# Performance work log

Measured on AMD Instinct MI355X. Metric: run time of the kernel, lower is better.

Reference implementation:

```python
import jax, jax.numpy as jnp
import numpy as np
import math

D_MODEL = 1024
N_HEAD = 16


def setup_inputs() -> dict:
    key = jax.random.key(0)
    ks = jax.random.split(key, 5)
    x = jax.random.normal(ks[0], (2, 2048, D_MODEL), dtype=jnp.float32)
    # Linear params (torch Linear: y = x @ W.T + b); store as [in, out] for einsum
    s1 = 1.0 / math.sqrt(D_MODEL)
    W_qkv = jax.random.uniform(ks[1], (D_MODEL, 3 * D_MODEL), jnp.float32, -s1, s1)
    b_qkv = jax.random.uniform(ks[2], (3 * D_MODEL,), jnp.float32, -s1, s1)
    W_out = jax.random.uniform(ks[3], (D_MODEL, D_MODEL), jnp.float32, -s1, s1)
    b_out = jax.random.uniform(ks[4], (D_MODEL,), jnp.float32, -s1, s1)
    return {"x": x, "W_qkv": W_qkv, "b_qkv": b_qkv, "W_out": W_out, "b_out": b_out}


def reference(x, W_qkv, b_qkv, W_out, b_out):
    B, L, D = x.shape
    H = N_HEAD
    hd = D // H
    qkv = x @ W_qkv + b_qkv                      # [B, L, 3D]
    q, k, v = jnp.split(qkv, 3, axis=-1)
    # [B, H, L, hd]
    q = q.reshape(B, L, H, hd).transpose(0, 2, 1, 3)
    k = k.reshape(B, L, H, hd).transpose(0, 2, 1, 3)
    v = v.reshape(B, L, H, hd).transpose(0, 2, 1, 3)
    scale = 1.0 / math.sqrt(hd)
    scores = jnp.einsum('bhqd,bhkd->bhqk', q, k) * scale   # [B, H, L, L]
    causal = jnp.tril(jnp.ones((L, L), dtype=bool))
    scores = jnp.where(causal, scores, jnp.float32(-jnp.inf))
    probs = jax.nn.softmax(scores, axis=-1)
    out = jnp.einsum('bhqk,bhkd->bhqd', probs, v)          # [B, H, L, hd]
    out = out.transpose(0, 2, 1, 3).reshape(B, L, D)
    out = out @ W_out + b_out
    return jnp.squeeze(out)
```

## Files before the change

kernel.cpp:

```cpp
#include <hip/hip_runtime.h>
#include <hip/hip_bf16.h>

#define SEQ    2048
#define NHEAD  16
#define HD     64
#define DMODEL 1024

using bf16 = __hip_bfloat16;
using short8 = __attribute__((ext_vector_type(8))) short;
using short4v = __attribute__((ext_vector_type(4))) short;
using f32x4  = __attribute__((ext_vector_type(4))) float;

__device__ __forceinline__ float fast_exp2(float x) {
  return __builtin_amdgcn_exp2f(x);
}
#define WAIT_LGKM0() __builtin_amdgcn_s_waitcnt(0xC07F)

__device__ __forceinline__ void gload_lds16(const bf16* g, bf16* l) {
  __builtin_amdgcn_global_load_lds(
      (const __attribute__((address_space(1))) void*)g,
      (__attribute__((address_space(3))) void*)l, 16, 0, 0);
}

__global__ void convert_k(const float* __restrict__ src, bf16* __restrict__ dst,
                          int n) {
  int i = (blockIdx.x * blockDim.x + threadIdx.x) * 8;
  if (i >= n) return;
  bf16 tmp[8];
  #pragma unroll
  for (int j = 0; j < 8; ++j) tmp[j] = __float2bfloat16(src[i + j]);
  *(short8*)&dst[i] = *(short8*)tmp;
}

__global__ void transpose_cvt_k(const float* __restrict__ in, bf16* __restrict__ out,
                                int R, int C) {
  __shared__ bf16 tile[32][33];
  int c0 = blockIdx.x * 32, r0 = blockIdx.y * 32;
  int tx = threadIdx.x & 31, ty = threadIdx.x >> 5;
  #pragma unroll
  for (int i = ty; i < 32; i += 8)
    tile[i][tx] = __float2bfloat16(in[(size_t)(r0 + i) * C + c0 + tx]);
  __syncthreads();
  #pragma unroll
  for (int i = ty; i < 32; i += 8)
    out[(size_t)(c0 + i) * R + r0 + tx] = tile[tx][i];
}

__global__ void transpose_v_k(const bf16* __restrict__ in, bf16* __restrict__ out) {
  __shared__ bf16 tile[32][33];
  const int bh = blockIdx.z;
  const bf16* ip = in  + (size_t)bh * SEQ * HD;
  bf16* op       = out + (size_t)bh * HD * SEQ;
  int c0 = blockIdx.x * 32, r0 = blockIdx.y * 32;
  int tx = threadIdx.x & 31, ty = threadIdx.x >> 5;
  #pragma unroll
  for (int i = ty; i < 32; i += 8)
    tile[i][tx] = ip[(size_t)(r0 + i) * HD + c0 + tx];
  __syncthreads();
  #pragma unroll
  for (int i = ty; i < 32; i += 8)
    op[(size_t)(c0 + i) * SEQ + r0 + tx] = tile[tx][i];
}

template <int MODE>
__global__ __launch_bounds__(256)
void gemm_bt(const bf16* __restrict__ A, const bf16* __restrict__ BT,
             const float* __restrict__ bias,
             bf16* __restrict__ out0, bf16* __restrict__ out1,
             bf16* __restrict__ out2, float* __restrict__ outf) {
  constexpr int K = 1024;
  __shared__ __align__(16) bf16 As[128 * 32];
  __shared__ __align__(16) bf16 Bs[128 * 32];
  const int tid = threadIdx.x;
  const int wave = tid >> 6, lane = tid & 63;
  const int quad = lane >> 4, l16 = lane & 15;
  const int waveM = (wave >> 1) * 64, waveN = (wave & 1) * 64;
  const int m0 = blockIdx.x * 128, n0 = blockIdx.y * 128;
  const int srow = (lane >> 2);
  const int scol = (lane & 3) * 8;

  const f32x4 zero4 = {0.f, 0.f, 0.f, 0.f};
  f32x4 acc[4][4];
  #pragma unroll
  for (int i = 0; i < 4; ++i)
    #pragma unroll
    for (int j = 0; j < 4; ++j) acc[i][j] = zero4;

  for (int k0 = 0; k0 < K; k0 += 32) {
    __syncthreads();
    #pragma unroll
    for (int half = 0; half < 2; ++half) {
      int grow = half * 64 + wave * 16 + srow;
      gload_lds16(&A [(size_t)(m0 + grow) * K + k0 + scol],
                  &As[(half * 64 + wave * 16) * 32]);
      gload_lds16(&BT[(size_t)(n0 + grow) * K + k0 + scol],
                  &Bs[(half * 64 + wave * 16) * 32]);
    }
    __syncthreads();
    short8 af[4], bfm[4];
    #pragma unroll
    for (int mt = 0; mt < 4; ++mt)
      af[mt] = *(const short8*)&As[(waveM + mt * 16 + l16) * 32 + quad * 8];
    #pragma unroll
    for (int nt = 0; nt < 4; ++nt)
      bfm[nt] = *(const short8*)&Bs[(waveN + nt * 16 + l16) * 32 + quad * 8];
    #pragma unroll
    for (int mt = 0; mt < 4; ++mt)
      #pragma unroll
      for (int nt = 0; nt < 4; ++nt)
        acc[mt][nt] = __builtin_amdgcn_mfma_f32_16x16x32_bf16(
            af[mt], bfm[nt], acc[mt][nt], 0, 0, 0);
  }

  #pragma unroll
  for (int nt = 0; nt < 4; ++nt) {
    int n = n0 + waveN + nt * 16 + l16;
    float bvv = bias[n];
    #pragma unroll
    for (int mt = 0; mt < 4; ++mt) {
      #pragma unroll
      for (int r = 0; r < 4; ++r) {
        int m = m0 + waveM + mt * 16 + quad * 4 + r;
        float v = acc[mt][nt][r] + bvv;
        if (MODE == 1) {
          outf[(size_t)m * 1024 + n] = v;
        } else {
          bf16 v16 = __float2bfloat16(v);
          int which = n >> 10, oo = n & 1023;
          int h = oo >> 6, c = oo & 63;
          int b = m >> 11, l = m & 2047;
          size_t idx = ((size_t)(b * NHEAD + h) * SEQ + l) * HD + c;
          if (which == 0)      out0[idx] = v16;
          else if (which == 1) out1[idx] = v16;
          else                 out2[idx] = v16;
        }
      }
    }
  }
}

__global__ __launch_bounds__(256)
void attn_k(const bf16* __restrict__ Q, const bf16* __restrict__ Kb,
            const bf16* __restrict__ VT, bf16* __restrict__ O) {
  __shared__ __align__(16) bf16 Ks[2 * 128 * 32];
  __shared__ __align__(16) bf16 Vs[4 * 64 * 32];
  __shared__ __align__(16) bf16 Plds[4][16][136];
  const int tid = threadIdx.x;
  const int wave = tid >> 6, lane = tid & 63;
  const int quad = lane >> 4, l16 = lane & 15;
  const int srow = lane >> 2, scol = (lane & 3) * 8;
  const int id = blockIdx.x;
  const int bh = id & 31, blkx = id >> 5;
  const int b = bh >> 4, h = bh & 15;

  const bf16* Qp = Q  + (size_t)bh * SEQ * HD;
  const bf16* Kp = Kb + (size_t)bh * SEQ * HD;
  const bf16* Vp = VT + (size_t)bh * HD * SEQ;

  const f32x4 zero4 = {0.f, 0.f, 0.f, 0.f};
  const float c = 0.18033688011112042f;
  const float mc = 8.0f * c;

  #pragma unroll
  for (int pass = 0; pass < 2; ++pass) {
    const int qt = pass ? (31 - blkx) : blkx;
    const int q0w = qt * 64 + wave * 16;
    const int q_lane = q0w + l16;
    const int ntiles = (qt + 2) >> 1;

    short8 qf0 = *(const short8*)&Qp[(size_t)(q0w + l16) * HD + quad * 8];
    short8 qf1 = *(const short8*)&Qp[(size_t)(q0w + l16) * HD + 32 + quad * 8];

    f32x4 oacc[4];
    #pragma unroll
    for (int dt = 0; dt < 4; ++dt) oacc[dt] = zero4;
    float l4[4] = {0.f, 0.f, 0.f, 0.f};

    for (int t = 0; t < ntiles; ++t) {
      const int k0 = t << 7;
      __syncthreads();
      #pragma unroll
      for (int i = 0; i < 2; ++i) {
        int r = wave * 32 + i * 16;
        #pragma unroll
        for (int hh = 0; hh < 2; ++hh)
          gload_lds16(&Kp[(size_t)(k0 + r + srow) * HD + hh * 32 + scol],
                      &Ks[hh * 4096 + r * 32]);
      }
      #pragma unroll
      for (int g = 0; g < 4; ++g)
        gload_lds16(&Vp[(size_t)(g * 16 + srow) * SEQ + k0 + wave * 32 + scol],
                    &Vs[wave * 2048 + g * 16 * 32]);
      __syncthreads();

      f32x4 s[8];
      #pragma unroll
      for (int g = 0; g < 8; ++g) {
        short8 ka = *(const short8*)&Ks[(g * 16 + l16) * 32 + quad * 8];
        short8 kb = *(const short8*)&Ks[4096 + (g * 16 + l16) * 32 + quad * 8];
        f32x4 sg = zero4;
        sg = __builtin_amdgcn_mfma_f32_16x16x32_bf16(ka, qf0, sg, 0, 0, 0);
        sg = __builtin_amdgcn_mfma_f32_16x16x32_bf16(kb, qf1, sg, 0, 0, 0);
        s[g] = sg;
      }

      if (t == ntiles - 1) {
        #pragma unroll
        for (int g = 0; g < 8; ++g)
          #pragma unroll
          for (int r = 0; r < 4; ++r) {
            int k = k0 + g * 16 + quad * 4 + r;
            s[g][r] = (k <= q_lane) ? s[g][r] : -__builtin_inff();
          }
      }

      #pragma unroll
      for (int g = 0; g < 8; ++g) {
        bf16 pb[4];
        #pragma unroll
        for (int r = 0; r < 4; ++r) {
          float p = fast_exp2(__builtin_fmaf(s[g][r], c, -mc));
          l4[r] += p;
          pb[r] = __float2bfloat16(p);
        }
        *(short4v*)&Plds[wave][l16][g * 16 + quad * 4] = *(short4v*)pb;
      }
      WAIT_LGKM0();

      short8 pf[4];
      #pragma unroll
      for (int ch = 0; ch < 4; ++ch)
        pf[ch] = *(const short8*)&Plds[wave][l16][ch * 32 + quad * 8];
      #pragma unroll
      for (int ch = 0; ch < 4; ++ch)
        #pragma unroll
        for (int dt = 0; dt < 4; ++dt) {
          short8 vf = *(const short8*)&Vs[ch * 2048 + (dt * 16 + l16) * 32 + quad * 8];
          oacc[dt] = __builtin_amdgcn_mfma_f32_16x16x32_bf16(vf, pf[ch], oacc[dt], 0, 0, 0);
        }
    }

    float l_i = (l4[0] + l4[1]) + (l4[2] + l4[3]);
    l_i += __shfl_xor(l_i, 16, 64);
    l_i += __shfl_xor(l_i, 32, 64);
    float inv = 1.f / l_i;

    #pragma unroll
    for (int dt = 0; dt < 4; ++dt) {
      bf16 ob[4];
      #pragma unroll
      for (int r = 0; r < 4; ++r) ob[r] = __float2bfloat16(oacc[dt][r] * inv);
      *(short4v*)&Plds[wave][l16][dt * 16 + quad * 4] = *(short4v*)ob;
    }
    WAIT_LGKM0();
    {
      int row = lane >> 2;
      int col = (lane & 3) * 16;
      short8 o0 = *(const short8*)&Plds[wave][row][col];
      short8 o1 = *(const short8*)&Plds[wave][row][col + 8];
      size_t base = ((size_t)(b * SEQ + q0w + row)) * DMODEL + h * HD + col;
      *(short8*)&O[base]     = o0;
      *(short8*)&O[base + 8] = o1;
    }
  }
}

extern "C" void kernel_launch(void* const* d_in, const int* in_sizes, int n_in,
                              void* d_out, int out_size, void* d_ws, size_t ws_size,
                              hipStream_t stream) {
  const float* x    = (const float*)d_in[0];
  const float* Wqkv = (const float*)d_in[1];
  const float* bqkv = (const float*)d_in[2];
  const float* Wout = (const float*)d_in[3];
  const float* bout = (const float*)d_in[4];
  float* out = (float*)d_out;

  char* ws = (char*)d_ws;
  const size_t MB = 1024 * 1024;
  char* big    = ws + 16384;
  bf16* Kbuf   = (bf16*)(big);
  bf16* VTb    = (bf16*)(big + 8 * MB);
  bf16* xb     = (bf16*)(big + 16 * MB);
  bf16* AO     = (bf16*)(big + 16 * MB);
  bf16* WqkvT  = (bf16*)(big + 24 * MB);
  bf16* WoutT  = (bf16*)(big + 30 * MB);
  bf16* Qb     = (bf16*)d_out;
  bf16* Vtmp   = (bf16*)((char*)d_out + 8 * MB);

  convert_k<<<(4194304 / 8 + 255) / 256, 256, 0, stream>>>(x, xb, 4194304);
  transpose_cvt_k<<<dim3(3072 / 32, 1024 / 32), 256, 0, stream>>>(Wqkv, WqkvT, 1024, 3072);
  transpose_cvt_k<<<dim3(1024 / 32, 1024 / 32), 256, 0, stream>>>(Wout, WoutT, 1024, 1024);
  gemm_bt<0><<<dim3(4096 / 128, 3072 / 128), 256, 0, stream>>>(
      xb, WqkvT, bqkv, Qb, Kbuf, Vtmp, nullptr);
  transpose_v_k<<<dim3(HD / 32, SEQ / 32, 32), 256, 0, stream>>>(Vtmp, VTb);
  attn_k<<<512, 256, 0, stream>>>(Qb, Kbuf, VTb, AO);
  gemm_bt<1><<<dim3(4096 / 128, 1024 / 128), 256, 0, stream>>>(
      AO, WoutT, bout, nullptr, nullptr, nullptr, out);
}
```

Before: 188.3 us.

## Fuse prep kernels, swizzle LDS reads, and enlarge attention query tiles

Merges the x conversion and both weight transpose kernels into a single prep launch to cut launch overhead. Adds an XOR swizzle to the LDS load and read columns in the GEMM and attention kernels to reduce bank conflicts. Restructures attention so each wave handles 32 query rows (two 16-row groups) against each 128-key tile, halving the grid to 256 blocks and reusing each K/V LDS load for twice the queries. The larger tile raises register pressure, and the smaller grid may leave CUs underused.

Result: slower. 192.4 us (+2.2%).

```diff
diff --git a/kernel.cpp b/kernel.cpp
--- a/kernel.cpp
+++ b/kernel.cpp
@@ -22,21 +22,30 @@
       (__attribute__((address_space(3))) void*)l, 16, 0, 0);
 }
 
-__global__ void convert_k(const float* __restrict__ src, bf16* __restrict__ dst,
-                          int n) {
-  int i = (blockIdx.x * blockDim.x + threadIdx.x) * 8;
-  if (i >= n) return;
-  bf16 tmp[8];
-  #pragma unroll
-  for (int j = 0; j < 8; ++j) tmp[j] = __float2bfloat16(src[i + j]);
-  *(short8*)&dst[i] = *(short8*)tmp;
-}
-
-__global__ void transpose_cvt_k(const float* __restrict__ in, bf16* __restrict__ out,
-                                int R, int C) {
+
+__global__ void prep_k(const float* __restrict__ x, bf16* __restrict__ xb,
+                       const float* __restrict__ Wqkv, bf16* __restrict__ WqkvT,
+                       const float* __restrict__ Wout, bf16* __restrict__ WoutT) {
   __shared__ bf16 tile[32][33];
-  int c0 = blockIdx.x * 32, r0 = blockIdx.y * 32;
-  int tx = threadIdx.x & 31, ty = threadIdx.x >> 5;
+  const int id = blockIdx.x, tid = threadIdx.x;
+  if (id < 2048) {
+    int i = (id * 256 + tid) * 8;
+    bf16 tmp[8];
+    #pragma unroll
+    for (int j = 0; j < 8; ++j) tmp[j] = __float2bfloat16(x[i + j]);
+    *(short8*)&xb[i] = *(short8*)tmp;
+    return;
+  }
+  const float* in; bf16* out; int R, C, tx32, ty32;
+  if (id < 2048 + 3072) {
+    int t = id - 2048; in = Wqkv; out = WqkvT; R = 1024; C = 3072;
+    tx32 = t % 96; ty32 = t / 96;
+  } else {
+    int t = id - 5120; in = Wout; out = WoutT; R = 1024; C = 1024;
+    tx32 = t % 32; ty32 = t / 32;
+  }
+  int c0 = tx32 * 32, r0 = ty32 * 32;
+  int tx = tid & 31, ty = tid >> 5;
   #pragma unroll
   for (int i = ty; i < 32; i += 8)
     tile[i][tx] = __float2bfloat16(in[(size_t)(r0 + i) * C + c0 + tx]);
@@ -77,7 +86,8 @@
   const int waveM = (wave >> 1) * 64, waveN = (wave & 1) * 64;
   const int m0 = blockIdx.x * 128, n0 = blockIdx.y * 128;
   const int srow = (lane >> 2);
-  const int scol = (lane & 3) * 8;
+  const int scol = (((lane & 3) ^ ((lane >> 3) & 3)) * 8);
+  const int q8   = (quad ^ ((l16 >> 1) & 3)) * 8;
 
   const f32x4 zero4 = {0.f, 0.f, 0.f, 0.f};
   f32x4 acc[4][4];
@@ -100,10 +110,10 @@
     short8 af[4], bfm[4];
     #pragma unroll
     for (int mt = 0; mt < 4; ++mt)
-      af[mt] = *(const short8*)&As[(waveM + mt * 16 + l16) * 32 + quad * 8];
+      af[mt] = *(const short8*)&As[(waveM + mt * 16 + l16) * 32 + q8];
     #pragma unroll
     for (int nt = 0; nt < 4; ++nt)
-      bfm[nt] = *(const short8*)&Bs[(waveN + nt * 16 + l16) * 32 + quad * 8];
+      bfm[nt] = *(const short8*)&Bs[(waveN + nt * 16 + l16) * 32 + q8];
     #pragma unroll
     for (int mt = 0; mt < 4; ++mt)
       #pragma unroll
@@ -142,13 +152,15 @@
 __global__ __launch_bounds__(256)
 void attn_k(const bf16* __restrict__ Q, const bf16* __restrict__ Kb,
             const bf16* __restrict__ VT, bf16* __restrict__ O) {
-  __shared__ __align__(16) bf16 Ks[2 * 128 * 32];
-  __shared__ __align__(16) bf16 Vs[4 * 64 * 32];
+  __shared__ __align__(16) bf16 Ks[2][128 * 32];
+  __shared__ __align__(16) bf16 Vs[4][64 * 32];
   __shared__ __align__(16) bf16 Plds[4][16][136];
   const int tid = threadIdx.x;
   const int wave = tid >> 6, lane = tid & 63;
   const int quad = lane >> 4, l16 = lane & 15;
-  const int srow = lane >> 2, scol = (lane & 3) * 8;
+  const int srow = lane >> 2;
+  const int scol = (((lane & 3) ^ ((lane >> 3) & 3)) * 8);
+  const int q8   = (quad ^ ((l16 >> 1) & 3)) * 8;
   const int id = blockIdx.x;
   const int bh = id & 31, blkx = id >> 5;
   const int b = bh >> 4, h = bh & 15;
@@ -161,47 +173,51 @@
   const float c = 0.18033688011112042f;
   const float mc = 8.0f * c;
 
-  #pragma unroll
   for (int pass = 0; pass < 2; ++pass) {
-    const int qt = pass ? (31 - blkx) : blkx;
-    const int q0w = qt * 64 + wave * 16;
-    const int q_lane = q0w + l16;
-    const int ntiles = (qt + 2) >> 1;
-
-    short8 qf0 = *(const short8*)&Qp[(size_t)(q0w + l16) * HD + quad * 8];
-    short8 qf1 = *(const short8*)&Qp[(size_t)(q0w + l16) * HD + 32 + quad * 8];
-
-    f32x4 oacc[4];
-    #pragma unroll
-    for (int dt = 0; dt < 4; ++dt) oacc[dt] = zero4;
-    float l4[4] = {0.f, 0.f, 0.f, 0.f};
+    const int qt = pass ? (15 - blkx) : blkx;
+    const int q0w = qt * 128 + wave * 32;
+    const int ntiles = qt + 1;
+
+    short8 qf[2][2];
+    #pragma unroll
+    for (int qg = 0; qg < 2; ++qg) {
+      qf[qg][0] = *(const short8*)&Qp[(size_t)(q0w + qg * 16 + l16) * HD + quad * 8];
+      qf[qg][1] = *(const short8*)&Qp[(size_t)(q0w + qg * 16 + l16) * HD + 32 + quad * 8];
+    }
+
+    f32x4 oacc[2][4];
+    #pragma unroll
+    for (int qg = 0; qg < 2; ++qg)
+      #pragma unroll
+      for (int dt = 0; dt < 4; ++dt) oacc[qg][dt] = zero4;
+    float l4[2][4] = {{0.f,0.f,0.f,0.f},{0.f,0.f,0.f,0.f}};
 
     for (int t = 0; t < ntiles; ++t) {
       const int k0 = t << 7;
       __syncthreads();
       #pragma unroll
-      for (int i = 0; i < 2; ++i) {
-        int r = wave * 32 + i * 16;
+      for (int i = 0; i < 2; ++i)
         #pragma unroll
         for (int hh = 0; hh < 2; ++hh)
-          gload_lds16(&Kp[(size_t)(k0 + r + srow) * HD + hh * 32 + scol],
-                      &Ks[hh * 4096 + r * 32]);
-      }
+          gload_lds16(&Kp[(size_t)(k0 + wave * 32 + i * 16 + srow) * HD + hh * 32 + scol],
+                      &Ks[hh][(wave * 32 + i * 16) * 32]);
       #pragma unroll
       for (int g = 0; g < 4; ++g)
         gload_lds16(&Vp[(size_t)(g * 16 + srow) * SEQ + k0 + wave * 32 + scol],
-                    &Vs[wave * 2048 + g * 16 * 32]);
+                    &Vs[wave][(g * 16) * 32]);
       __syncthreads();
 
-      f32x4 s[8];
+      f32x4 s0[8], s1[8];
       #pragma unroll
       for (int g = 0; g < 8; ++g) {
-        short8 ka = *(const short8*)&Ks[(g * 16 + l16) * 32 + quad * 8];
-        short8 kb = *(const short8*)&Ks[4096 + (g * 16 + l16) * 32 + quad * 8];
-        f32x4 sg = zero4;
-        sg = __builtin_amdgcn_mfma_f32_16x16x32_bf16(ka, qf0, sg, 0, 0, 0);
-        sg = __builtin_amdgcn_mfma_f32_16x16x32_bf16(kb, qf1, sg, 0, 0, 0);
-        s[g] = sg;
+        short8 ka = *(const short8*)&Ks[0][(g * 16 + l16) * 32 + q8];
+        short8 kb = *(const short8*)&Ks[1][(g * 16 + l16) * 32 + q8];
+        f32x4 a = zero4, bb = zero4;
+        a  = __builtin_amdgcn_mfma_f32_16x16x32_bf16(ka, qf[0][0], a, 0, 0, 0);
+        a  = __builtin_amdgcn_mfma_f32_16x16x32_bf16(kb, qf[0][1], a, 0, 0, 0);
+        bb = __builtin_amdgcn_mfma_f32_16x16x32_bf16(ka, qf[1][0], bb, 0, 0, 0);
+        bb = __builtin_amdgcn_mfma_f32_16x16x32_bf16(kb, qf[1][1], bb, 0, 0, 0);
+        s0[g] = a; s1[g] = bb;
       }
 
       if (t == ntiles - 1) {
@@ -210,57 +226,61 @@
           #pragma unroll
           for (int r = 0; r < 4; ++r) {
             int k = k0 + g * 16 + quad * 4 + r;
-            s[g][r] = (k <= q_lane) ? s[g][r] : -__builtin_inff();
+            s0[g][r] = (k <= q0w + l16)      ? s0[g][r] : -__builtin_inff();
+            s1[g][r] = (k <= q0w + 16 + l16) ? s1[g][r] : -__builtin_inff();
           }
       }
 
       #pragma unroll
-      for (int g = 0; g < 8; ++g) {
-        bf16 pb[4];
-        #pragma unroll
-        for (int r = 0; r < 4; ++r) {
-          float p = fast_exp2(__builtin_fmaf(s[g][r], c, -mc));
-          l4[r] += p;
-          pb[r] = __float2bfloat16(p);
+      for (int qg = 0; qg < 2; ++qg) {
+        f32x4* s = qg ? s1 : s0;
+        #pragma unroll
+        for (int g = 0; g < 8; ++g) {
+          bf16 pb[4];
+          #pragma unroll
+          for (int r = 0; r < 4; ++r) {
+            float p = fast_exp2(__builtin_fmaf(s[g][r], c, -mc));
+            l4[qg][r] += p;
+            pb[r] = __float2bfloat16(p);
+          }
+          *(short4v*)&Plds[wave][l16][g * 16 + quad * 4] = *(short4v*)pb;
         }
-        *(short4v*)&Plds[wave][l16][g * 16 + quad * 4] = *(short4v*)pb;
+        WAIT_LGKM0();
+        #pragma unroll
+        for (int ch = 0; ch < 4; ++ch) {
+          short8 pf = *(const short8*)&Plds[wave][l16][ch * 32 + quad * 8];
+          #pragma unroll
+          for (int dt = 0; dt < 4; ++dt) {
+            short8 vf = *(const short8*)&Vs[ch][(dt * 16 + l16) * 32 + q8];
+            oacc[qg][dt] = __builtin_amdgcn_mfma_f32_16x16x32_bf16(
+                vf, pf, oacc[qg][dt], 0, 0, 0);
+          }
+        }
+      }
+    }
+
+    #pragma unroll
+    for (int qg = 0; qg < 2; ++qg) {
+      float l_i = (l4[qg][0] + l4[qg][1]) + (l4[qg][2] + l4[qg][3]);
+      l_i += __shfl_xor(l_i, 16, 64);
+      l_i += __shfl_xor(l_i, 32, 64);
+      float inv = 1.f / l_i;
+      #pragma unroll
+      for (int dt = 0; dt < 4; ++dt) {
+        bf16 ob[4];
+        #pragma unroll
+        for (int r = 0; r < 4; ++r) ob[r] = __float2bfloat16(oacc[qg][dt][r] * inv);
+        *(short4v*)&Plds[wave][l16][dt * 16 + quad * 4] = *(short4v*)ob;
       }
       WAIT_LGKM0();
-
-      short8 pf[4];
-      #pragma unroll
-      for (int ch = 0; ch < 4; ++ch)
-        pf[ch] = *(const short8*)&Plds[wave][l16][ch * 32 + quad * 8];
-      #pragma unroll
-      for (int ch = 0; ch < 4; ++ch)
-        #pragma unroll
-        for (int dt = 0; dt < 4; ++dt) {
-          short8 vf = *(const short8*)&Vs[ch * 2048 + (dt * 16 + l16) * 32 + quad * 8];
-          oacc[dt] = __builtin_amdgcn_mfma_f32_16x16x32_bf16(vf, pf[ch], oacc[dt], 0, 0, 0);
-        }
-    }
-
-    float l_i = (l4[0] + l4[1]) + (l4[2] + l4[3]);
-    l_i += __shfl_xor(l_i, 16, 64);
-    l_i += __shfl_xor(l_i, 32, 64);
-    float inv = 1.f / l_i;
-
-    #pragma unroll
-    for (int dt = 0; dt < 4; ++dt) {
-      bf16 ob[4];
-      #pragma unroll
-      for (int r = 0; r < 4; ++r) ob[r] = __float2bfloat16(oacc[dt][r] * inv);
-      *(short4v*)&Plds[wave][l16][dt * 16 + quad * 4] = *(short4v*)ob;
-    }
-    WAIT_LGKM0();
-    {
       int row = lane >> 2;
       int col = (lane & 3) * 16;
       short8 o0 = *(const short8*)&Plds[wave][row][col];
       short8 o1 = *(const short8*)&Plds[wave][row][col + 8];
-      size_t base = ((size_t)(b * SEQ + q0w + row)) * DMODEL + h * HD + col;
+      size_t base = ((size_t)(b * SEQ + q0w + qg * 16 + row)) * DMODEL + h * HD + col;
       *(short8*)&O[base]     = o0;
       *(short8*)&O[base + 8] = o1;
+      WAIT_LGKM0();
     }
   }
 }
@@ -287,13 +307,11 @@
   bf16* Qb     = (bf16*)d_out;
   bf16* Vtmp   = (bf16*)((char*)d_out + 8 * MB);
 
-  convert_k<<<(4194304 / 8 + 255) / 256, 256, 0, stream>>>(x, xb, 4194304);
-  transpose_cvt_k<<<dim3(3072 / 32, 1024 / 32), 256, 0, stream>>>(Wqkv, WqkvT, 1024, 3072);
-  transpose_cvt_k<<<dim3(1024 / 32, 1024 / 32), 256, 0, stream>>>(Wout, WoutT, 1024, 1024);
+  prep_k<<<6144, 256, 0, stream>>>(x, xb, Wqkv, WqkvT, Wout, WoutT);
   gemm_bt<0><<<dim3(4096 / 128, 3072 / 128), 256, 0, stream>>>(
       xb, WqkvT, bqkv, Qb, Kbuf, Vtmp, nullptr);
   transpose_v_k<<<dim3(HD / 32, SEQ / 32, 32), 256, 0, stream>>>(Vtmp, VTb);
-  attn_k<<<512, 256, 0, stream>>>(Qb, Kbuf, VTb, AO);
+  attn_k<<<256, 256, 0, stream>>>(Qb, Kbuf, VTb, AO);
   gemm_bt<1><<<dim3(4096 / 128, 1024 / 128), 256, 0, stream>>>(
       AO, WoutT, bout, nullptr, nullptr, nullptr, out);
 }
```
